# Performance work log

Hardware: AMD Instinct MI355X
Metric: run time of the kernel (lower is better)

The kernel has to match this reference:

```python
import jax, jax.numpy as jnp
import numpy as np

DIM = 1024
NUM_HEADS = 16
HEAD_DIM = DIM // NUM_HEADS
SCALE = HEAD_DIM ** -0.5


def setup_inputs() -> dict:
    key = jax.random.key(0)
    k1, k2, k3, k4 = jax.random.split(key, 4)
    B, N = 2, 2048
    x = jax.random.normal(k1, (B, N, DIM), dtype=jnp.float32)
    # qkv: Linear(dim, 3*dim, bias=False); torch stores weight as [out, in]
    W_qkv = jax.random.normal(k2, (3 * DIM, DIM), dtype=jnp.float32) * (DIM ** -0.5)
    # proj: Linear(dim, dim, bias=True)
    W_proj = jax.random.normal(k3, (DIM, DIM), dtype=jnp.float32) * (DIM ** -0.5)
    b_proj = jax.random.normal(k4, (DIM,), dtype=jnp.float32) * 0.01
    return {"x": x, "W_qkv": W_qkv, "W_proj": W_proj, "b_proj": b_proj}


def reference(x, W_qkv, W_proj, b_proj):
    B, N, C = x.shape
    H, D = NUM_HEADS, HEAD_DIM
    # qkv projection: [B,N,3C] -> [3,B,H,N,D]
    qkv = jnp.einsum('bnc,oc->bno', x, W_qkv)
    qkv = qkv.reshape(B, N, 3, H, D).transpose(2, 0, 3, 1, 4)
    q, k, v = qkv[0] * SCALE, qkv[1], qkv[2]
    # full attention matrix [B,H,N,N] (faithful to manual impl)
    attn = jnp.einsum('bhqd,bhkd->bhqk', q, k)
    attn = jax.nn.softmax(attn, axis=-1)
    # dropout p=0.0 -> identity (eval semantics)
    out = jnp.einsum('bhqk,bhkd->bhqd', attn, v)  # [B,H,N,D]
    out = out.transpose(0, 2, 1, 3).reshape(B, N, C)
    out = jnp.einsum('bnc,oc->bno', out, W_proj) + b_proj
    return out
```

## Files before the change

### kernel.cpp

```cpp
#include <hip/hip_runtime.h>
#include <math.h>

#define BATCH 2
#define NTOK  2048
#define DIMC  1024
#define NH    16
#define HD    64
#define SOFT_K2 0.18033688011112042f

typedef __bf16 bf16;
typedef __attribute__((ext_vector_type(8))) __bf16 bf16x8;
typedef __attribute__((ext_vector_type(4))) __bf16 bf16x4;
typedef __attribute__((ext_vector_type(4))) float f32x4;

__device__ __forceinline__ void load_lds16(const void* g, void* l) {
    __builtin_amdgcn_global_load_lds(
        (const __attribute__((address_space(1))) void*)g,
        (__attribute__((address_space(3))) void*)l, 16, 0, 0);
}
__device__ __forceinline__ f32x4 mfma16(bf16x8 a, bf16x8 b, f32x4 c) {
    return __builtin_amdgcn_mfma_f32_16x16x32_bf16(a, b, c, 0, 0, 0);
}

__global__ __launch_bounds__(256) void cast3(
    const float* __restrict__ x,  const float* __restrict__ w1, const float* __restrict__ w2,
    bf16* __restrict__ xb, bf16* __restrict__ w1b, bf16* __restrict__ w2b)
{
    int blk = blockIdx.x;
    const float* src; bf16* dst; size_t base;
    if (blk < 4096)      { src = x;  dst = xb;  base = (size_t)blk * 1024; }
    else if (blk < 7168) { src = w1; dst = w1b; base = (size_t)(blk - 4096) * 1024; }
    else                 { src = w2; dst = w2b; base = (size_t)(blk - 7168) * 1024; }
    size_t i = base + (size_t)threadIdx.x * 4;
    float4 v = *(const float4*)(src + i);
    bf16x4 r;
    r[0] = (bf16)v.x; r[1] = (bf16)v.y; r[2] = (bf16)v.z; r[3] = (bf16)v.w;
    *(bf16x4*)(dst + i) = r;
}

template<int BM, int BN, bool OUT_BF16>
__global__ __launch_bounds__(256) void gemm_bt(
    const bf16* __restrict__ A, const bf16* __restrict__ B,
    const float* __restrict__ bias, void* __restrict__ Cout,
    int M, int N, int K)
{
    __shared__ __align__(16) bf16 As[BM * 32];
    __shared__ __align__(16) bf16 Bs[BN * 32];

    constexpr int WM = BM / 2, WN = BN / 2;
    constexpr int TA = BM / 64, TB = BN / 64;

    const int tid  = threadIdx.x;
    const int w    = tid >> 6, lane = tid & 63;
    const int wm   = w & 1,  wn = w >> 1;
    const int m0   = blockIdx.y * BM, n0 = blockIdx.x * BN;
    const int lm   = lane & 15, quad = lane >> 4;

    const bf16* Ag[TA]; const bf16* Bg[TB];
#pragma unroll
    for (int t = 0; t < TA; ++t) {
        int c = t * 256 + tid;
        Ag[t] = A + (size_t)(m0 + (c % BM)) * K + (c / BM) * 8;
    }
#pragma unroll
    for (int t = 0; t < TB; ++t) {
        int c = t * 256 + tid;
        Bg[t] = B + (size_t)(n0 + (c % BN)) * K + (c / BN) * 8;
    }

    f32x4 acc[WM / 16][WN / 16];
    f32x4 z4 = {0.f, 0.f, 0.f, 0.f};
#pragma unroll
    for (int i = 0; i < WM / 16; ++i)
#pragma unroll
        for (int j = 0; j < WN / 16; ++j) acc[i][j] = z4;

    for (int kt = 0; kt < K; kt += 32) {
        __syncthreads();
#pragma unroll
        for (int t = 0; t < TA; ++t)
            load_lds16(Ag[t] + kt, As + (t * 256 + w * 64) * 8);
#pragma unroll
        for (int t = 0; t < TB; ++t)
            load_lds16(Bg[t] + kt, Bs + (t * 256 + w * 64) * 8);
        __syncthreads();

        bf16x8 af[WM / 16], bf_[WN / 16];
#pragma unroll
        for (int mi = 0; mi < WM / 16; ++mi)
            af[mi] = *(const bf16x8*)(As + (quad * BM + wm * WM + mi * 16 + lm) * 8);
#pragma unroll
        for (int ni = 0; ni < WN / 16; ++ni)
            bf_[ni] = *(const bf16x8*)(Bs + (quad * BN + wn * WN + ni * 16 + lm) * 8);
#pragma unroll
        for (int mi = 0; mi < WM / 16; ++mi)
#pragma unroll
            for (int ni = 0; ni < WN / 16; ++ni)
                acc[mi][ni] = mfma16(af[mi], bf_[ni], acc[mi][ni]);
    }

#pragma unroll
    for (int ni = 0; ni < WN / 16; ++ni) {
        const int col = n0 + wn * WN + ni * 16 + lm;
        const float bi = (!OUT_BF16 && bias) ? bias[col] : 0.0f;
#pragma unroll
        for (int mi = 0; mi < WM / 16; ++mi)
#pragma unroll
            for (int r = 0; r < 4; ++r) {
                const int row = m0 + wm * WM + mi * 16 + quad * 4 + r;
                const float v = acc[mi][ni][r] + bi;
                if (OUT_BF16) ((bf16*)Cout)[(size_t)row * N + col] = (bf16)v;
                else          ((float*)Cout)[(size_t)row * N + col] = v;
            }
    }
}

__global__ __launch_bounds__(256) void transpose_v(
    const bf16* __restrict__ qkv, bf16* __restrict__ Vt)
{
    __shared__ bf16 T[64][72];
    const int n0 = blockIdx.x * 64, h = blockIdx.y, b = blockIdx.z;
    const int tid = threadIdx.x;
    const int a = tid >> 2;
    const int c = tid & 3;
#pragma unroll
    for (int it = 0; it < 4; ++it) {
        int d0 = (c + it * 4) * 4;
        bf16x4 v = *(const bf16x4*)(qkv + (size_t)(b * NTOK + n0 + a) * (3 * DIMC)
                                    + 2 * DIMC + h * HD + d0);
        T[d0 + 0][a] = v[0]; T[d0 + 1][a] = v[1];
        T[d0 + 2][a] = v[2]; T[d0 + 3][a] = v[3];
    }
    __syncthreads();
#pragma unroll
    for (int it = 0; it < 4; ++it) {
        int n1 = (c + it * 4) * 4;
        bf16x4 o;
        o[0] = T[a][n1]; o[1] = T[a][n1 + 1]; o[2] = T[a][n1 + 2]; o[3] = T[a][n1 + 3];
        *(bf16x4*)(Vt + ((size_t)((b * NH + h) * HD + a)) * NTOK + n0 + n1) = o;
    }
}

__global__ __launch_bounds__(256) void attn_mfma(
    const bf16* __restrict__ qkv,
    const bf16* __restrict__ Vt,
    bf16* __restrict__ att)
{
    __shared__ __align__(16) bf16 Qs[64 * 64];
    __shared__ __align__(16) bf16 Ks[2][64 * 64];
    __shared__ __align__(16) bf16 Vs[2][64 * 64];
    __shared__ __align__(16) bf16 Ps[64 * 72];

    const int n0 = blockIdx.x * 64, h = blockIdx.y, b = blockIdx.z;
    const int tid = threadIdx.x, w = tid >> 6, lane = tid & 63;
    const int lm = lane & 15, quad = lane >> 4;

    const size_t rs = (size_t)(3 * DIMC);
    const bf16* qbase  = qkv + (size_t)b * NTOK * rs + h * HD;
    const bf16* kbase  = qbase + DIMC;
    const bf16* vtbase = Vt + ((size_t)(b * NH + h) * HD) * NTOK;

    const int l0 = (w * 2 + 0) * 64 + lane, l1 = (w * 2 + 1) * 64 + lane;
    const bf16* kg0 = kbase + (size_t)(l0 & 63) * rs + (l0 >> 6) * 8;
    const bf16* kg1 = kbase + (size_t)(l1 & 63) * rs + (l1 >> 6) * 8;
    const bf16* vg0 = vtbase + (size_t)(l0 & 63) * NTOK + (l0 >> 6) * 8;
    const bf16* vg1 = vtbase + (size_t)(l1 & 63) * NTOK + (l1 >> 6) * 8;

    load_lds16(qbase + (size_t)(n0 + (l0 & 63)) * rs + (l0 >> 6) * 8, Qs + (w * 2 + 0) * 512);
    load_lds16(qbase + (size_t)(n0 + (l1 & 63)) * rs + (l1 >> 6) * 8, Qs + (w * 2 + 1) * 512);
    load_lds16(kg0, Ks[0] + (w * 2 + 0) * 512);
    load_lds16(kg1, Ks[0] + (w * 2 + 1) * 512);
    load_lds16(vg0, Vs[0] + (w * 2 + 0) * 512);
    load_lds16(vg1, Vs[0] + (w * 2 + 1) * 512);

    f32x4 O[4];
    f32x4 z4 = {0.f, 0.f, 0.f, 0.f};
#pragma unroll
    for (int ni = 0; ni < 4; ++ni) O[ni] = z4;
    float lsum[4] = {0.f, 0.f, 0.f, 0.f};

    const int NT = NTOK / 64;
    for (int t = 0; t < NT; ++t) {
        const int buf = t & 1;
        __syncthreads();
        if (t + 1 < NT) {
            const size_t koff = (size_t)(t + 1) * 64 * rs;
            const size_t voff = (size_t)(t + 1) * 64;
            load_lds16(kg0 + koff, Ks[buf ^ 1] + (w * 2 + 0) * 512);
            load_lds16(kg1 + koff, Ks[buf ^ 1] + (w * 2 + 1) * 512);
            load_lds16(vg0 + voff, Vs[buf ^ 1] + (w * 2 + 0) * 512);
            load_lds16(vg1 + voff, Vs[buf ^ 1] + (w * 2 + 1) * 512);
        }

        f32x4 S[4];
#pragma unroll
        for (int ni = 0; ni < 4; ++ni) S[ni] = z4;
#pragma unroll
        for (int s2 = 0; s2 < 2; ++s2) {
            bf16x8 aq = *(const bf16x8*)(Qs + ((s2 * 4 + quad) * 64 + w * 16 + lm) * 8);
#pragma unroll
            for (int ni = 0; ni < 4; ++ni) {
                bf16x8 bk = *(const bf16x8*)(Ks[buf] + ((s2 * 4 + quad) * 64 + ni * 16 + lm) * 8);
                S[ni] = mfma16(aq, bk, S[ni]);
            }
        }

#pragma unroll
        for (int ni = 0; ni < 4; ++ni)
#pragma unroll
            for (int r = 0; r < 4; ++r) {
                const float p = __builtin_amdgcn_exp2f(S[ni][r] * SOFT_K2);
                Ps[(w * 16 + quad * 4 + r) * 72 + ni * 16 + lm] = (bf16)p;
                lsum[r] += p;
            }

#pragma unroll
        for (int s2 = 0; s2 < 2; ++s2) {
            bf16x8 ap = *(const bf16x8*)(Ps + (w * 16 + lm) * 72 + s2 * 32 + quad * 8);
#pragma unroll
            for (int ni = 0; ni < 4; ++ni) {
                bf16x8 bv = *(const bf16x8*)(Vs[buf] + ((s2 * 4 + quad) * 64 + ni * 16 + lm) * 8);
                O[ni] = mfma16(ap, bv, O[ni]);
            }
        }
    }

#pragma unroll
    for (int r = 0; r < 4; ++r) {
#pragma unroll
        for (int msk = 1; msk < 16; msk <<= 1) lsum[r] += __shfl_xor(lsum[r], msk);
    }

#pragma unroll
    for (int r = 0; r < 4; ++r) {
        const float invl = 1.0f / lsum[r];
        const size_t row = (size_t)(b * NTOK + n0 + w * 16 + quad * 4 + r);
#pragma unroll
        for (int ni = 0; ni < 4; ++ni)
            att[row * DIMC + h * HD + ni * 16 + lm] = (bf16)(O[ni][r] * invl);
    }
}

extern "C" void kernel_launch(void* const* d_in, const int* in_sizes, int n_in,
                              void* d_out, int out_size, void* d_ws, size_t ws_size,
                              hipStream_t stream)
{
    const float* x      = (const float*)d_in[0];
    const float* W_qkv  = (const float*)d_in[1];
    const float* W_proj = (const float*)d_in[2];
    const float* b_proj = (const float*)d_in[3];
    float* out = (float*)d_out;

    char* ws = (char*)d_ws;
    bf16* xb   = (bf16*)ws;
    bf16* w1b  = (bf16*)(ws + (8u  << 20));
    bf16* w2b  = (bf16*)(ws + (14u << 20));
    bf16* qkvb = (bf16*)(ws + (16u << 20));
    bf16* vt   = (bf16*)(ws + (40u << 20));
    bf16* attb = (bf16*)(ws + (48u << 20));

    const int M = BATCH * NTOK;

    cast3<<<8192, 256, 0, stream>>>(x, W_qkv, W_proj, xb, w1b, w2b);

    gemm_bt<128, 128, true><<<dim3((3 * DIMC) / 128, M / 128), 256, 0, stream>>>(
        xb, w1b, nullptr, qkvb, M, 3 * DIMC, DIMC);

    transpose_v<<<dim3(NTOK / 64, NH, BATCH), 256, 0, stream>>>(qkvb, vt);

    attn_mfma<<<dim3(NTOK / 64, NH, BATCH), 256, 0, stream>>>(qkvb, vt, attb);

    gemm_bt<64, 128, false><<<dim3(DIMC / 128, M / 64), 256, 0, stream>>>(
        attb, w2b, b_proj, out, M, DIMC, DIMC);
}
```

Before: 276.0 us.

## Process 128 query rows per attention block to reuse K/V tiles

Each attention block now handles 128 query rows instead of 64, with every wave computing two 16-row groups that share each loaded K and V fragment. This halves the number of K/V tile loads from global memory and the LDS fragment reads per MFMA. In exchange the grid shrinks to 512 blocks, and register and LDS use per block roughly double, which may lower occupancy. Launch bounds are set to request two blocks per CU.

```diff
diff --git a/kernel.cpp b/kernel.cpp
--- a/kernel.cpp
+++ b/kernel.cpp
@@ -141,17 +141,17 @@
     }
 }
 
-__global__ __launch_bounds__(256) void attn_mfma(
+__global__ __launch_bounds__(256, 2) void attn_mfma(
     const bf16* __restrict__ qkv,
     const bf16* __restrict__ Vt,
     bf16* __restrict__ att)
 {
-    __shared__ __align__(16) bf16 Qs[64 * 64];
+    __shared__ __align__(16) bf16 Qs[128 * 64];
     __shared__ __align__(16) bf16 Ks[2][64 * 64];
     __shared__ __align__(16) bf16 Vs[2][64 * 64];
-    __shared__ __align__(16) bf16 Ps[64 * 72];
-
-    const int n0 = blockIdx.x * 64, h = blockIdx.y, b = blockIdx.z;
+    __shared__ __align__(16) bf16 Ps[128 * 72];
+
+    const int n0 = blockIdx.x * 128, h = blockIdx.y, b = blockIdx.z;
     const int tid = threadIdx.x, w = tid >> 6, lane = tid & 63;
     const int lm = lane & 15, quad = lane >> 4;
 
@@ -159,6 +159,13 @@
     const bf16* qbase  = qkv + (size_t)b * NTOK * rs + h * HD;
     const bf16* kbase  = qbase + DIMC;
     const bf16* vtbase = Vt + ((size_t)(b * NH + h) * HD) * NTOK;
+
+#pragma unroll
+    for (int t = 0; t < 4; ++t) {
+        const int l = t * 256 + tid;
+        load_lds16(qbase + (size_t)(n0 + (l & 127)) * rs + (l >> 7) * 8,
+                   Qs + (t * 256 + w * 64) * 8);
+    }
 
     const int l0 = (w * 2 + 0) * 64 + lane, l1 = (w * 2 + 1) * 64 + lane;
     const bf16* kg0 = kbase + (size_t)(l0 & 63) * rs + (l0 >> 6) * 8;
@@ -166,18 +173,18 @@
     const bf16* vg0 = vtbase + (size_t)(l0 & 63) * NTOK + (l0 >> 6) * 8;
     const bf16* vg1 = vtbase + (size_t)(l1 & 63) * NTOK + (l1 >> 6) * 8;
 
-    load_lds16(qbase + (size_t)(n0 + (l0 & 63)) * rs + (l0 >> 6) * 8, Qs + (w * 2 + 0) * 512);
-    load_lds16(qbase + (size_t)(n0 + (l1 & 63)) * rs + (l1 >> 6) * 8, Qs + (w * 2 + 1) * 512);
     load_lds16(kg0, Ks[0] + (w * 2 + 0) * 512);
     load_lds16(kg1, Ks[0] + (w * 2 + 1) * 512);
     load_lds16(vg0, Vs[0] + (w * 2 + 0) * 512);
     load_lds16(vg1, Vs[0] + (w * 2 + 1) * 512);
 
-    f32x4 O[4];
+    f32x4 O[2][4];
     f32x4 z4 = {0.f, 0.f, 0.f, 0.f};
 #pragma unroll
-    for (int ni = 0; ni < 4; ++ni) O[ni] = z4;
-    float lsum[4] = {0.f, 0.f, 0.f, 0.f};
+    for (int g = 0; g < 2; ++g)
+#pragma unroll
+        for (int ni = 0; ni < 4; ++ni) O[g][ni] = z4;
+    float lsum[2][4] = {{0.f, 0.f, 0.f, 0.f}, {0.f, 0.f, 0.f, 0.f}};
 
     const int NT = NTOK / 64;
     for (int t = 0; t < NT; ++t) {
@@ -192,53 +199,66 @@
             load_lds16(vg1 + voff, Vs[buf ^ 1] + (w * 2 + 1) * 512);
         }
 
-        f32x4 S[4];
-#pragma unroll
-        for (int ni = 0; ni < 4; ++ni) S[ni] = z4;
+        f32x4 S[2][4];
+#pragma unroll
+        for (int g = 0; g < 2; ++g)
+#pragma unroll
+            for (int ni = 0; ni < 4; ++ni) S[g][ni] = z4;
 #pragma unroll
         for (int s2 = 0; s2 < 2; ++s2) {
-            bf16x8 aq = *(const bf16x8*)(Qs + ((s2 * 4 + quad) * 64 + w * 16 + lm) * 8);
+            bf16x8 aq0 = *(const bf16x8*)(Qs + ((s2 * 4 + quad) * 128 + w * 32 + lm) * 8);
+            bf16x8 aq1 = *(const bf16x8*)(Qs + ((s2 * 4 + quad) * 128 + w * 32 + 16 + lm) * 8);
 #pragma unroll
             for (int ni = 0; ni < 4; ++ni) {
                 bf16x8 bk = *(const bf16x8*)(Ks[buf] + ((s2 * 4 + quad) * 64 + ni * 16 + lm) * 8);
-                S[ni] = mfma16(aq, bk, S[ni]);
+                S[0][ni] = mfma16(aq0, bk, S[0][ni]);
+                S[1][ni] = mfma16(aq1, bk, S[1][ni]);
             }
         }
 
 #pragma unroll
-        for (int ni = 0; ni < 4; ++ni)
-#pragma unroll
-            for (int r = 0; r < 4; ++r) {
-                const float p = __builtin_amdgcn_exp2f(S[ni][r] * SOFT_K2);
-                Ps[(w * 16 + quad * 4 + r) * 72 + ni * 16 + lm] = (bf16)p;
-                lsum[r] += p;
-            }
+        for (int g = 0; g < 2; ++g)
+#pragma unroll
+            for (int ni = 0; ni < 4; ++ni)
+#pragma unroll
+                for (int r = 0; r < 4; ++r) {
+                    const float p = __builtin_amdgcn_exp2f(S[g][ni][r] * SOFT_K2);
+                    Ps[(w * 32 + g * 16 + quad * 4 + r) * 72 + ni * 16 + lm] = (bf16)p;
+                    lsum[g][r] += p;
+                }
 
 #pragma unroll
         for (int s2 = 0; s2 < 2; ++s2) {
-            bf16x8 ap = *(const bf16x8*)(Ps + (w * 16 + lm) * 72 + s2 * 32 + quad * 8);
+            bf16x8 ap0 = *(const bf16x8*)(Ps + (w * 32 + lm) * 72 + s2 * 32 + quad * 8);
+            bf16x8 ap1 = *(const bf16x8*)(Ps + (w * 32 + 16 + lm) * 72 + s2 * 32 + quad * 8);
 #pragma unroll
             for (int ni = 0; ni < 4; ++ni) {
                 bf16x8 bv = *(const bf16x8*)(Vs[buf] + ((s2 * 4 + quad) * 64 + ni * 16 + lm) * 8);
-                O[ni] = mfma16(ap, bv, O[ni]);
+                O[0][ni] = mfma16(ap0, bv, O[0][ni]);
+                O[1][ni] = mfma16(ap1, bv, O[1][ni]);
             }
         }
     }
 
 #pragma unroll
-    for (int r = 0; r < 4; ++r) {
-#pragma unroll
-        for (int msk = 1; msk < 16; msk <<= 1) lsum[r] += __shfl_xor(lsum[r], msk);
-    }
-
-#pragma unroll
-    for (int r = 0; r < 4; ++r) {
-        const float invl = 1.0f / lsum[r];
-        const size_t row = (size_t)(b * NTOK + n0 + w * 16 + quad * 4 + r);
-#pragma unroll
-        for (int ni = 0; ni < 4; ++ni)
-            att[row * DIMC + h * HD + ni * 16 + lm] = (bf16)(O[ni][r] * invl);
-    }
+    for (int g = 0; g < 2; ++g)
+#pragma unroll
+        for (int r = 0; r < 4; ++r) {
+#pragma unroll
+            for (int msk = 1; msk < 16; msk <<= 1)
+                lsum[g][r] += __shfl_xor(lsum[g][r], msk);
+        }
+
+#pragma unroll
+    for (int g = 0; g < 2; ++g)
+#pragma unroll
+        for (int r = 0; r < 4; ++r) {
+            const float invl = 1.0f / lsum[g][r];
+            const size_t row = (size_t)(b * NTOK + n0 + w * 32 + g * 16 + quad * 4 + r);
+#pragma unroll
+            for (int ni = 0; ni < 4; ++ni)
+                att[row * DIMC + h * HD + ni * 16 + lm] = (bf16)(O[g][ni][r] * invl);
+        }
 }
 
 extern "C" void kernel_launch(void* const* d_in, const int* in_sizes, int n_in,
@@ -268,7 +288,7 @@
 
     transpose_v<<<dim3(NTOK / 64, NH, BATCH), 256, 0, stream>>>(qkvb, vt);
 
-    attn_mfma<<<dim3(NTOK / 64, NH, BATCH), 256, 0, stream>>>(qkvb, vt, attb);
+    attn_mfma<<<dim3(NTOK / 128, NH, BATCH), 256, 0, stream>>>(qkvb, vt, attb);
 
     gemm_bt<64, 128, false><<<dim3(DIMC / 128, M / 64), 256, 0, stream>>>(
         attb, w2b, b_proj, out, M, DIMC, DIMC);
```

Measured after the change: 230.7 us. 1.2x faster.
